# Kernel optimization log

Measured on AMD Instinct MI355X. Metric: run time of the kernel, lower is better.

## Reference

```python
import jax, jax.numpy as jnp
import numpy as np

D_MODEL = 1024
NUM_HEADS = 16
DEPTH = D_MODEL // NUM_HEADS
MAX_SEQ = 2048
B, S = 2, 2048


def setup_inputs() -> dict:
    key = jax.random.key(0)
    ks = jax.random.split(key, 12)
    scale = 1.0 / np.sqrt(D_MODEL)
    inp = {
        'q': jax.random.normal(ks[0], (B, S, D_MODEL), jnp.float32),
        'k': jax.random.normal(ks[1], (B, S, D_MODEL), jnp.float32),
        'v': jax.random.normal(ks[2], (B, S, D_MODEL), jnp.float32),
        'mask': jnp.zeros((B, 1, S, S), jnp.float32),
        'wq_w': jax.random.normal(ks[3], (D_MODEL, D_MODEL), jnp.float32) * scale,
        'wq_b': jnp.zeros((D_MODEL,), jnp.float32),
        'wk_w': jax.random.normal(ks[4], (D_MODEL, D_MODEL), jnp.float32) * scale,
        'wk_b': jnp.zeros((D_MODEL,), jnp.float32),
        'wv_w': jax.random.normal(ks[5], (D_MODEL, D_MODEL), jnp.float32) * scale,
        'wv_b': jnp.zeros((D_MODEL,), jnp.float32),
        'dense_w': jax.random.normal(ks[6], (D_MODEL, D_MODEL), jnp.float32) * scale,
        'dense_b': jnp.zeros((D_MODEL,), jnp.float32),
        'rel_bias': jax.random.normal(ks[7], (2 * MAX_SEQ - 1, NUM_HEADS), jnp.float32),
    }
    return inp


def _split_heads(x):
    # [B, S, D_MODEL] -> [B, H, S, depth]
    b, s, _ = x.shape
    return x.reshape(b, s, NUM_HEADS, DEPTH).transpose(0, 2, 1, 3)


def reference(q, k, v, mask, wq_w, wq_b, wk_w, wk_b, wv_w, wv_b, dense_w, dense_b, rel_bias):
    b, s, _ = q.shape
    # torch Linear: y = x @ W.T + b
    qh = _split_heads(q @ wq_w.T + wq_b)
    kh = _split_heads(k @ wk_w.T + wk_b)
    vh = _split_heads(v @ wv_w.T + wv_b)
    logits = jnp.einsum('bhqd,bhkd->bhqk', qh, kh) / jnp.sqrt(jnp.float32(DEPTH))
    # relative position bias gather
    pos = jnp.arange(s)
    idx = jnp.clip(pos[:, None] - pos[None, :] + MAX_SEQ - 1, 0, 2 * MAX_SEQ - 2)  # [S, S]
    pos_bias = rel_bias[idx]                      # [S, S, H]
    pos_bias = pos_bias.transpose(2, 0, 1)[None]  # [1, H, S, S]
    logits = logits + pos_bias + mask * (-1e9)
    attn = jax.nn.softmax(logits, axis=-1)        # dropout is identity in eval
    out = jnp.einsum('bhqk,bhkd->bhqd', attn, vh)
    out = out.transpose(0, 2, 1, 3).reshape(b, s, D_MODEL)
    out = out @ dense_w.T + dense_b
    return out, attn
```

## Files before the change

kernel.cpp:

```cpp
#include <hip/hip_runtime.h>

typedef _Float16 f16x8 __attribute__((ext_vector_type(8)));
typedef _Float16 f16x4 __attribute__((ext_vector_type(4)));
typedef float f32x4 __attribute__((ext_vector_type(4)));
typedef unsigned short u16x8 __attribute__((ext_vector_type(8)));
typedef unsigned int u32;

#define MFMA16H(a, b, c) __builtin_amdgcn_mfma_f32_16x16x32_f16(a, b, c, 0, 0, 0)

#if __has_builtin(__builtin_amdgcn_exp2f)
#define EXP2F(x) __builtin_amdgcn_exp2f(x)
#else
#define EXP2F(x) exp2f(x)
#endif

#define LOG2E 1.44269504088896340736f
#define SHIFT2 5.0f

__device__ __forceinline__ unsigned short f2bf(float x) {
  unsigned u = __float_as_uint(x);
  u += 0x7FFF + ((u >> 16) & 1);
  return (unsigned short)(u >> 16);
}
__device__ __forceinline__ float bf2f(unsigned short h) {
  return __uint_as_float(((unsigned)h) << 16);
}
__device__ __forceinline__ f16x8 ldh8(const _Float16* p) {
  return *reinterpret_cast<const f16x8*>(p);
}
__device__ __forceinline__ u16x8 ldu8(const unsigned short* p) {
  return *reinterpret_cast<const u16x8*>(p);
}

__global__ __launch_bounds__(256) void prep_kernel(
    const float* __restrict__ q, const float* __restrict__ k, const float* __restrict__ v,
    const float* __restrict__ wq, const float* __restrict__ wk, const float* __restrict__ wv,
    const float* __restrict__ dwt, const float* __restrict__ mask,
    _Float16* __restrict__ qf, _Float16* __restrict__ kf, _Float16* __restrict__ vf,
    _Float16* __restrict__ wqf, _Float16* __restrict__ wkf, _Float16* __restrict__ wvf,
    _Float16* __restrict__ dwf, unsigned short* __restrict__ mperm) {
  if (blockIdx.x < 2048) {
    const int blk = blockIdx.x;
    const int kt = blk & 31, bq = blk >> 5;
    const int b = bq >> 5, qt = bq & 31;
    const int lane = threadIdx.x;
    const int w = lane >> 6, lg = (lane >> 4) & 3, lr = lane & 15;
    const int q0 = qt * 64;
    const float cs = -1e9f * LOG2E;
    unsigned short vals[16];
#pragma unroll
    for (int c = 0; c < 4; ++c)
#pragma unroll
      for (int r = 0; r < 4; ++r) {
        const int qr = q0 + w * 16 + lg * 4 + r;
        const int kc = kt * 64 + c * 16 + lr;
        vals[c * 4 + r] = f2bf(mask[((size_t)b * 2048 + qr) * 2048 + kc] * cs);
      }
    uint4* out = reinterpret_cast<uint4*>(mperm) + ((size_t)blk * 256 + lane) * 2;
    out[0] = *reinterpret_cast<uint4*>(&vals[0]);
    out[1] = *reinterpret_cast<uint4*>(&vals[8]);
    return;
  }
  const int i = (blockIdx.x - 2048) * 256 + threadIdx.x;
  const int r = i >> 18;
  const int j = i & 262143;
  const float* src;
  _Float16* dst;
  int off = 0;
  if (r < 4)       { src = q;   dst = qf;  off = r * 262144; }
  else if (r < 8)  { src = k;   dst = kf;  off = (r - 4) * 262144; }
  else if (r < 12) { src = v;   dst = vf;  off = (r - 8) * 262144; }
  else if (r == 12){ src = wq;  dst = wqf; }
  else if (r == 13){ src = wk;  dst = wkf; }
  else if (r == 14){ src = wv;  dst = wvf; }
  else             { src = dwt; dst = dwf; }
  const int g = off + j;
  float4 x = reinterpret_cast<const float4*>(src)[g];
  f16x4 h;
  h[0] = (_Float16)x.x; h[1] = (_Float16)x.y;
  h[2] = (_Float16)x.z; h[3] = (_Float16)x.w;
  reinterpret_cast<f16x4*>(dst)[g] = h;
}

__device__ __forceinline__ void gemm_body(
    int t, int mode, const _Float16* __restrict__ A, const _Float16* __restrict__ B,
    const float* __restrict__ bias, _Float16* __restrict__ out_h, float* __restrict__ out_f,
    _Float16* As, _Float16* Bs) {
  const int tid = threadIdx.x;
  const int tm = t & 31, tn = t >> 5;
  const int m0 = tm * 128, n0 = tn * 128;
  const int w = tid >> 6, l = tid & 63, lg = l >> 4, lr = l & 15;
  const int wr = w >> 1, wc = w & 1;
  const int srow = tid >> 2, scol = (tid & 3) * 8;

  f32x4 acc[4][4] = {};

  for (int kt = 0; kt < 32; ++kt) {
    const int k0 = kt * 32;
    uint4 ra[2], rb[2];
#pragma unroll
    for (int it = 0; it < 2; ++it) {
      const int row = it * 64 + srow;
      ra[it] = *reinterpret_cast<const uint4*>(A + (size_t)(m0 + row) * 1024 + k0 + scol);
      rb[it] = *reinterpret_cast<const uint4*>(B + (size_t)(n0 + row) * 1024 + k0 + scol);
    }
    __syncthreads();
#pragma unroll
    for (int it = 0; it < 2; ++it) {
      const int eo = (it * 256 + tid) * 8;
      *reinterpret_cast<uint4*>(As + eo) = ra[it];
      *reinterpret_cast<uint4*>(Bs + eo) = rb[it];
    }
    __syncthreads();

    f16x8 fa[4], fb[4];
#pragma unroll
    for (int i = 0; i < 4; ++i) {
      fa[i] = ldh8(As + (wr * 64 + i * 16 + lr) * 32 + lg * 8);
      fb[i] = ldh8(Bs + (wc * 64 + i * 16 + lr) * 32 + lg * 8);
    }
#pragma unroll
    for (int i = 0; i < 4; ++i)
#pragma unroll
      for (int j = 0; j < 4; ++j)
        acc[i][j] = MFMA16H(fa[i], fb[j], acc[i][j]);
  }

#pragma unroll
  for (int i = 0; i < 4; ++i) {
    const int mrow = m0 + wr * 64 + i * 16 + lg * 4;
#pragma unroll
    for (int j = 0; j < 4; ++j) {
      const int ncol = n0 + wc * 64 + j * 16 + lr;
      const float bv = bias[ncol];
#pragma unroll
      for (int r = 0; r < 4; ++r) {
        const int m = mrow + r;
        const float v = acc[i][j][r] + bv;
        if (mode == 2) {
          out_f[(size_t)m * 1024 + ncol] = v;
        } else {
          const int bb = m >> 11, s = m & 2047, hh = ncol >> 6, d = ncol & 63;
          if (mode == 0)
            out_h[((size_t)(bb * 16 + hh) * 2048 + s) * 64 + d] = (_Float16)v;
          else
            out_h[((size_t)(bb * 16 + hh) * 64 + d) * 2048 + s] = (_Float16)v;
        }
      }
    }
  }
}

__global__ __launch_bounds__(256, 3) void proj_gemm_kernel(
    const _Float16* __restrict__ qf, const _Float16* __restrict__ kf, const _Float16* __restrict__ vf,
    const _Float16* __restrict__ wqf, const _Float16* __restrict__ wkf, const _Float16* __restrict__ wvf,
    const float* __restrict__ bq, const float* __restrict__ bk, const float* __restrict__ bv,
    _Float16* __restrict__ qhf, _Float16* __restrict__ khf, _Float16* __restrict__ vhT) {
  __shared__ __align__(16) _Float16 As[128 * 32];
  __shared__ __align__(16) _Float16 Bs[128 * 32];
  const int mode = blockIdx.x >> 8;
  const int t = blockIdx.x & 255;
  if (mode == 0)      gemm_body(t, 0, qf, wqf, bq, qhf, nullptr, As, Bs);
  else if (mode == 1) gemm_body(t, 0, kf, wkf, bk, khf, nullptr, As, Bs);
  else                gemm_body(t, 1, vf, wvf, bv, vhT, nullptr, As, Bs);
}

__global__ __launch_bounds__(256) void dense_gemm_kernel(
    const _Float16* __restrict__ A, const _Float16* __restrict__ Bw,
    const float* __restrict__ bias, float* __restrict__ out_f) {
  __shared__ __align__(16) _Float16 As[128 * 32];
  __shared__ __align__(16) _Float16 Bs[128 * 32];
  gemm_body(blockIdx.x, 2, A, Bw, bias, nullptr, out_f, As, Bs);
}

__global__ __launch_bounds__(128) void attn_sums_kernel(
    const _Float16* __restrict__ qh, const _Float16* __restrict__ kh,
    const float* __restrict__ rel_bias, const unsigned short* __restrict__ mperm,
    float* __restrict__ sums2) {
  __shared__ float rb2[2080];
  const int bid = blockIdx.x;
  const int wg = ((bid & 7) << 9) | (bid >> 3);
  const int half = wg & 1;
  const int qt = (wg >> 1) & 63;
  const int bh = wg >> 7;
  const int b = bh >> 4, h = bh & 15;
  const int q0 = qt * 32;
  const int tid = threadIdx.x;
  const int w2 = tid >> 6, l = tid & 63, lg = l >> 4, lr = l & 15;

  for (int t = tid; t < 2079; t += 128)
    rb2[t] = rel_bias[(q0 + t) * 16 + h] * LOG2E - SHIFT2;

  const size_t bh_off = (size_t)bh * 2048 * 64;
  const _Float16* qhb = qh + bh_off;
  const _Float16* khb = kh + bh_off;
  const int qt64 = qt >> 1;
  const int wp = (qt & 1) * 2 + w2;
  const int lanep = wp * 64 + lg * 16 + lr;
  const unsigned short* mpb =
      mperm + (((size_t)(b * 32 + qt64) * 32) * 256 + lanep) * 16;

  f16x8 qf[2];
  {
    const size_t qrow = (size_t)(q0 + w2 * 16 + lr) * 64;
    qf[0] = ldh8(qhb + qrow + lg * 8);
    qf[1] = ldh8(qhb + qrow + 32 + lg * 8);
  }
  __syncthreads();

  const int qbase = w2 * 16 + lg * 4;
  const float c1 = 0.125f * LOG2E;
  float sacc[4] = {0.f, 0.f, 0.f, 0.f};

  const int kt0 = half * 16;
#pragma unroll 2
  for (int kt = kt0; kt < kt0 + 16; ++kt) {
    u16x8 m0v = ldu8(mpb + (size_t)kt * 4096);
    u16x8 m1v = ldu8(mpb + (size_t)kt * 4096 + 8);
#pragma unroll
    for (int c = 0; c < 4; ++c) {
      const int kc = kt * 64 + c * 16 + lr;
      const _Float16* kr = khb + (size_t)kc * 64 + lg * 8;
      f32x4 acc = {};
      acc = MFMA16H(qf[0], ldh8(kr), acc);
      acc = MFMA16H(qf[1], ldh8(kr + 32), acc);
#pragma unroll
      for (int r = 0; r < 4; ++r) {
        const float mbf = bf2f((c < 2) ? (unsigned short)m0v[(c & 1) * 4 + r]
                                       : (unsigned short)m1v[(c & 1) * 4 + r]);
        const float l2 = fmaf(acc[r], c1, rb2[qbase + r - kc + 2047]) + mbf;
        sacc[r] += EXP2F(l2);
      }
    }
  }

#pragma unroll
  for (int r = 0; r < 4; ++r) {
    float s = sacc[r];
    s += __shfl_xor(s, 1);
    s += __shfl_xor(s, 2);
    s += __shfl_xor(s, 4);
    s += __shfl_xor(s, 8);
    if (lr == 0)
      sums2[((size_t)bh * 2048 + q0 + qbase + r) * 2 + half] = s;
  }
}

__global__ __launch_bounds__(128) void attn_emit_kernel(
    const _Float16* __restrict__ qh, const _Float16* __restrict__ kh,
    const _Float16* __restrict__ vT,
    const float* __restrict__ rel_bias, const unsigned short* __restrict__ mperm,
    const float* __restrict__ sums2, float* __restrict__ attn_out,
    _Float16* __restrict__ o_h) {
  __shared__ float rb2[2080];
  __shared__ __align__(16) _Float16 p16t[2][32 * 76];

  const int bid = blockIdx.x;
  const int wg = ((bid & 7) << 8) | (bid >> 3);
  const int qt = wg & 63;
  const int bh = wg >> 6;
  const int b = bh >> 4, h = bh & 15;
  const int q0 = qt * 32;
  const int tid = threadIdx.x;
  const int w2 = tid >> 6, l = tid & 63, lg = l >> 4, lr = l & 15;

  for (int t = tid; t < 2079; t += 128)
    rb2[t] = rel_bias[(q0 + t) * 16 + h] * LOG2E - SHIFT2;

  const size_t bh_off = (size_t)bh * 2048 * 64;
  const _Float16* qhb = qh + bh_off;
  const _Float16* khb = kh + bh_off;
  const _Float16* vTb = vT + bh_off;
  const int qt64 = qt >> 1;
  const int wp = (qt & 1) * 2 + w2;
  const int lanep = wp * 64 + lg * 16 + lr;
  const unsigned short* mpb =
      mperm + (((size_t)(b * 32 + qt64) * 32) * 256 + lanep) * 16;
  float* attn_bh = attn_out + (size_t)bh * 2048 * 2048;

  const int qbase = w2 * 16 + lg * 4;

  f16x8 qf[2];
  {
    const size_t qrow = (size_t)(q0 + w2 * 16 + lr) * 64;
    qf[0] = ldh8(qhb + qrow + lg * 8);
    qf[1] = ldh8(qhb + qrow + 32 + lg * 8);
  }
  float inv[4];
  {
    const float* sp = sums2 + ((size_t)bh * 2048 + q0 + qbase) * 2;
    float4 s0 = *reinterpret_cast<const float4*>(sp);
    float4 s1 = *reinterpret_cast<const float4*>(sp + 4);
    inv[0] = 1.0f / (s0.x + s0.y);
    inv[1] = 1.0f / (s0.z + s0.w);
    inv[2] = 1.0f / (s1.x + s1.y);
    inv[3] = 1.0f / (s1.z + s1.w);
  }
  __syncthreads();

  const float c1 = 0.125f * LOG2E;
  f32x4 acc_o[4] = {};
  const int sg = l >> 4, sc = (l & 15) * 4;

#pragma unroll 2
  for (int kt = 0; kt < 32; ++kt) {
    _Float16* tile = p16t[kt & 1];
    u16x8 m0v = ldu8(mpb + (size_t)kt * 4096);
    u16x8 m1v = ldu8(mpb + (size_t)kt * 4096 + 8);
#pragma unroll
    for (int c = 0; c < 4; ++c) {
      const int kc = kt * 64 + c * 16 + lr;
      const _Float16* kr = khb + (size_t)kc * 64 + lg * 8;
      f32x4 acc = {};
      acc = MFMA16H(qf[0], ldh8(kr), acc);
      acc = MFMA16H(qf[1], ldh8(kr + 32), acc);
#pragma unroll
      for (int r = 0; r < 4; ++r) {
        const float mbf = bf2f((c < 2) ? (unsigned short)m0v[(c & 1) * 4 + r]
                                       : (unsigned short)m1v[(c & 1) * 4 + r]);
        const float l2 = fmaf(acc[r], c1, rb2[qbase + r - kc + 2047]) + mbf;
        tile[(qbase + r) * 76 + c * 16 + lr] = (_Float16)(EXP2F(l2) * inv[r]);
      }
    }
    f16x8 pf0 = ldh8(tile + (w2 * 16 + lr) * 76 + lg * 8);
    f16x8 pf1 = ldh8(tile + (w2 * 16 + lr) * 76 + 32 + lg * 8);
#pragma unroll
    for (int n = 0; n < 4; ++n) {
      const _Float16* vr = vTb + (size_t)(n * 16 + lr) * 2048 + kt * 64 + lg * 8;
      acc_o[n] = MFMA16H(pf0, ldh8(vr), acc_o[n]);
      acc_o[n] = MFMA16H(pf1, ldh8(vr + 32), acc_o[n]);
    }
#pragma unroll
    for (int i = 0; i < 4; ++i) {
      const int row = w2 * 16 + i * 4 + sg;
      f16x4 pw = *reinterpret_cast<const f16x4*>(tile + row * 76 + sc);
      float4 o;
      o.x = (float)pw[0]; o.y = (float)pw[1];
      o.z = (float)pw[2]; o.w = (float)pw[3];
      *reinterpret_cast<float4*>(attn_bh + (size_t)(q0 + row) * 2048 + kt * 64 + sc) = o;
    }
  }

#pragma unroll
  for (int n = 0; n < 4; ++n)
#pragma unroll
    for (int r = 0; r < 4; ++r) {
      const int qr = q0 + qbase + r;
      const int d = n * 16 + lr;
      o_h[((size_t)(b * 2048 + qr) * 16 + h) * 64 + d] = (_Float16)acc_o[n][r];
    }
}

extern "C" void kernel_launch(void* const* d_in, const int* in_sizes, int n_in,
                              void* d_out, int out_size, void* d_ws, size_t ws_size,
                              hipStream_t stream) {
  const float* q = (const float*)d_in[0];
  const float* k = (const float*)d_in[1];
  const float* v = (const float*)d_in[2];
  const float* mask = (const float*)d_in[3];
  const float* wq_w = (const float*)d_in[4];
  const float* wq_b = (const float*)d_in[5];
  const float* wk_w = (const float*)d_in[6];
  const float* wk_b = (const float*)d_in[7];
  const float* wv_w = (const float*)d_in[8];
  const float* wv_b = (const float*)d_in[9];
  const float* dw = (const float*)d_in[10];
  const float* db = (const float*)d_in[11];
  const float* rel = (const float*)d_in[12];

  char* ws = (char*)d_ws;
  _Float16* qf_in = (_Float16*)(ws + 0);
  _Float16* kf_in = (_Float16*)(ws + 8388608);
  _Float16* vf_in = (_Float16*)(ws + 16777216);
  _Float16* wqf   = (_Float16*)(ws + 25165824);
  _Float16* wkf   = (_Float16*)(ws + 27262976);
  _Float16* wvf   = (_Float16*)(ws + 29360128);
  _Float16* dwf   = (_Float16*)(ws + 31457280);
  _Float16* qhf   = (_Float16*)(ws + 33554432);
  _Float16* khf   = (_Float16*)(ws + 41943040);
  _Float16* vhT   = (_Float16*)(ws + 50331648);
  _Float16* o_h   = (_Float16*)(ws + 58720256);
  float* sums2    = (float*)(ws + 67108864);
  unsigned short* mperm = (unsigned short*)(ws + 67633152);

  float* out = (float*)d_out;
  float* attn_out = out + 4194304;

  prep_kernel<<<18432, 256, 0, stream>>>(q, k, v, wq_w, wk_w, wv_w, dw, mask,
                                         qf_in, kf_in, vf_in, wqf, wkf, wvf, dwf, mperm);

  proj_gemm_kernel<<<768, 256, 0, stream>>>(qf_in, kf_in, vf_in, wqf, wkf, wvf,
                                            wq_b, wk_b, wv_b, qhf, khf, vhT);

  attn_sums_kernel<<<4096, 128, 0, stream>>>(qhf, khf, rel, mperm, sums2);

  attn_emit_kernel<<<2048, 128, 0, stream>>>(qhf, khf, vhT, rel, mperm,
                                             sums2, attn_out, o_h);

  dense_gemm_kernel<<<256, 256, 0, stream>>>(o_h, dwf, db, out);
}
```

Baseline: 681.4 us.

## Precompute permuted fp16 relative-bias tiles and split attention emit across key halves

Relative-position bias is precomputed in the prep kernel into per-head, per-diagonal fp16 tiles laid out in MFMA lane order. Both attention kernels add these tiles to the fp16 mask tiles instead of staging a float bias table in LDS, which removes LDS fills and one sync per block. The emit kernel now uses 256-thread blocks over 64 query rows, each handling one half of the keys, and writes partial outputs to two buffers. The dense GEMM sums those buffers while loading A. The risks are lost precision from fp16 bias, mask and partial outputs, the removed SHIFT2 offset, and extra workspace traffic.

```diff
diff --git a/kernel.cpp b/kernel.cpp
--- a/kernel.cpp
+++ b/kernel.cpp
@@ -3,7 +3,6 @@
 typedef _Float16 f16x8 __attribute__((ext_vector_type(8)));
 typedef _Float16 f16x4 __attribute__((ext_vector_type(4)));
 typedef float f32x4 __attribute__((ext_vector_type(4)));
-typedef unsigned short u16x8 __attribute__((ext_vector_type(8)));
 typedef unsigned int u32;
 
 #define MFMA16H(a, b, c) __builtin_amdgcn_mfma_f32_16x16x32_f16(a, b, c, 0, 0, 0)
@@ -15,53 +14,58 @@
 #endif
 
 #define LOG2E 1.44269504088896340736f
-#define SHIFT2 5.0f
-
-__device__ __forceinline__ unsigned short f2bf(float x) {
-  unsigned u = __float_as_uint(x);
-  u += 0x7FFF + ((u >> 16) & 1);
-  return (unsigned short)(u >> 16);
-}
-__device__ __forceinline__ float bf2f(unsigned short h) {
-  return __uint_as_float(((unsigned)h) << 16);
-}
+
 __device__ __forceinline__ f16x8 ldh8(const _Float16* p) {
   return *reinterpret_cast<const f16x8*>(p);
-}
-__device__ __forceinline__ u16x8 ldu8(const unsigned short* p) {
-  return *reinterpret_cast<const u16x8*>(p);
 }
 
 __global__ __launch_bounds__(256) void prep_kernel(
     const float* __restrict__ q, const float* __restrict__ k, const float* __restrict__ v,
     const float* __restrict__ wq, const float* __restrict__ wk, const float* __restrict__ wv,
-    const float* __restrict__ dwt, const float* __restrict__ mask,
+    const float* __restrict__ dwt, const float* __restrict__ mask, const float* __restrict__ rel,
     _Float16* __restrict__ qf, _Float16* __restrict__ kf, _Float16* __restrict__ vf,
     _Float16* __restrict__ wqf, _Float16* __restrict__ wkf, _Float16* __restrict__ wvf,
-    _Float16* __restrict__ dwf, unsigned short* __restrict__ mperm) {
+    _Float16* __restrict__ dwf, _Float16* __restrict__ mperm, _Float16* __restrict__ rperm) {
+  const int lane = threadIdx.x;
+  const int w = lane >> 6, lg = (lane >> 4) & 3, lr = lane & 15;
   if (blockIdx.x < 2048) {
     const int blk = blockIdx.x;
     const int kt = blk & 31, bq = blk >> 5;
     const int b = bq >> 5, qt = bq & 31;
-    const int lane = threadIdx.x;
-    const int w = lane >> 6, lg = (lane >> 4) & 3, lr = lane & 15;
     const int q0 = qt * 64;
     const float cs = -1e9f * LOG2E;
-    unsigned short vals[16];
+    _Float16 vals[16];
 #pragma unroll
     for (int c = 0; c < 4; ++c)
 #pragma unroll
       for (int r = 0; r < 4; ++r) {
         const int qr = q0 + w * 16 + lg * 4 + r;
         const int kc = kt * 64 + c * 16 + lr;
-        vals[c * 4 + r] = f2bf(mask[((size_t)b * 2048 + qr) * 2048 + kc] * cs);
+        vals[c * 4 + r] =
+            (_Float16)fmaxf(mask[((size_t)b * 2048 + qr) * 2048 + kc] * cs, -60000.0f);
       }
     uint4* out = reinterpret_cast<uint4*>(mperm) + ((size_t)blk * 256 + lane) * 2;
     out[0] = *reinterpret_cast<uint4*>(&vals[0]);
     out[1] = *reinterpret_cast<uint4*>(&vals[8]);
     return;
   }
-  const int i = (blockIdx.x - 2048) * 256 + threadIdx.x;
+  if (blockIdx.x < 3056) {
+    const int blk = blockIdx.x - 2048;
+    const int h = blk / 63, d = blk % 63;
+    _Float16 vals[16];
+#pragma unroll
+    for (int c = 0; c < 4; ++c)
+#pragma unroll
+      for (int r = 0; r < 4; ++r) {
+        const int idx = (d - 31) * 64 + (w * 16 + lg * 4 + r) - (c * 16 + lr) + 2047;
+        vals[c * 4 + r] = (_Float16)(rel[idx * 16 + h] * LOG2E);
+      }
+    uint4* out = reinterpret_cast<uint4*>(rperm) + ((size_t)blk * 256 + lane) * 2;
+    out[0] = *reinterpret_cast<uint4*>(&vals[0]);
+    out[1] = *reinterpret_cast<uint4*>(&vals[8]);
+    return;
+  }
+  const int i = (blockIdx.x - 3056) * 256 + threadIdx.x;
   const int r = i >> 18;
   const int j = i & 262143;
   const float* src;
@@ -76,10 +80,10 @@
   else             { src = dwt; dst = dwf; }
   const int g = off + j;
   float4 x = reinterpret_cast<const float4*>(src)[g];
-  f16x4 h;
-  h[0] = (_Float16)x.x; h[1] = (_Float16)x.y;
-  h[2] = (_Float16)x.z; h[3] = (_Float16)x.w;
-  reinterpret_cast<f16x4*>(dst)[g] = h;
+  f16x4 h4;
+  h4[0] = (_Float16)x.x; h4[1] = (_Float16)x.y;
+  h4[2] = (_Float16)x.z; h4[3] = (_Float16)x.w;
+  reinterpret_cast<f16x4*>(dst)[g] = h4;
 }
 
 __device__ __forceinline__ void gemm_body(
@@ -166,18 +170,71 @@
 }
 
 __global__ __launch_bounds__(256) void dense_gemm_kernel(
-    const _Float16* __restrict__ A, const _Float16* __restrict__ Bw,
-    const float* __restrict__ bias, float* __restrict__ out_f) {
+    const _Float16* __restrict__ A0, const _Float16* __restrict__ A1,
+    const _Float16* __restrict__ Bw, const float* __restrict__ bias,
+    float* __restrict__ out_f) {
   __shared__ __align__(16) _Float16 As[128 * 32];
   __shared__ __align__(16) _Float16 Bs[128 * 32];
-  gemm_body(blockIdx.x, 2, A, Bw, bias, nullptr, out_f, As, Bs);
-}
-
-__global__ __launch_bounds__(128) void attn_sums_kernel(
+  const int tid = threadIdx.x;
+  const int t = blockIdx.x;
+  const int tm = t & 31, tn = t >> 5;
+  const int m0 = tm * 128, n0 = tn * 128;
+  const int w = tid >> 6, l = tid & 63, lg = l >> 4, lr = l & 15;
+  const int wr = w >> 1, wc = w & 1;
+  const int srow = tid >> 2, scol = (tid & 3) * 8;
+
+  f32x4 acc[4][4] = {};
+
+  for (int kt = 0; kt < 32; ++kt) {
+    const int k0 = kt * 32;
+    f16x8 ra[2], rb[2];
+#pragma unroll
+    for (int it = 0; it < 2; ++it) {
+      const int row = it * 64 + srow;
+      const size_t ga = (size_t)(m0 + row) * 1024 + k0 + scol;
+      ra[it] = ldh8(A0 + ga) + ldh8(A1 + ga);
+      rb[it] = ldh8(Bw + (size_t)(n0 + row) * 1024 + k0 + scol);
+    }
+    __syncthreads();
+#pragma unroll
+    for (int it = 0; it < 2; ++it) {
+      const int eo = (it * 256 + tid) * 8;
+      *reinterpret_cast<f16x8*>(As + eo) = ra[it];
+      *reinterpret_cast<f16x8*>(Bs + eo) = rb[it];
+    }
+    __syncthreads();
+
+    f16x8 fa[4], fb[4];
+#pragma unroll
+    for (int i = 0; i < 4; ++i) {
+      fa[i] = ldh8(As + (wr * 64 + i * 16 + lr) * 32 + lg * 8);
+      fb[i] = ldh8(Bs + (wc * 64 + i * 16 + lr) * 32 + lg * 8);
+    }
+#pragma unroll
+    for (int i = 0; i < 4; ++i)
+#pragma unroll
+      for (int j = 0; j < 4; ++j)
+        acc[i][j] = MFMA16H(fa[i], fb[j], acc[i][j]);
+  }
+
+#pragma unroll
+  for (int i = 0; i < 4; ++i) {
+    const int mrow = m0 + wr * 64 + i * 16 + lg * 4;
+#pragma unroll
+    for (int j = 0; j < 4; ++j) {
+      const int ncol = n0 + wc * 64 + j * 16 + lr;
+      const float bv = bias[ncol];
+#pragma unroll
+      for (int r = 0; r < 4; ++r)
+        out_f[(size_t)(mrow + r) * 1024 + ncol] = acc[i][j][r] + bv;
+    }
+  }
+}
+
+__global__ __launch_bounds__(128, 8) void attn_sums_kernel(
     const _Float16* __restrict__ qh, const _Float16* __restrict__ kh,
-    const float* __restrict__ rel_bias, const unsigned short* __restrict__ mperm,
+    const _Float16* __restrict__ mperm, const _Float16* __restrict__ rperm,
     float* __restrict__ sums2) {
-  __shared__ float rb2[2080];
   const int bid = blockIdx.x;
   const int wg = ((bid & 7) << 9) | (bid >> 3);
   const int half = wg & 1;
@@ -188,25 +245,21 @@
   const int tid = threadIdx.x;
   const int w2 = tid >> 6, l = tid & 63, lg = l >> 4, lr = l & 15;
 
-  for (int t = tid; t < 2079; t += 128)
-    rb2[t] = rel_bias[(q0 + t) * 16 + h] * LOG2E - SHIFT2;
-
   const size_t bh_off = (size_t)bh * 2048 * 64;
   const _Float16* qhb = qh + bh_off;
   const _Float16* khb = kh + bh_off;
   const int qt64 = qt >> 1;
   const int wp = (qt & 1) * 2 + w2;
   const int lanep = wp * 64 + lg * 16 + lr;
-  const unsigned short* mpb =
-      mperm + (((size_t)(b * 32 + qt64) * 32) * 256 + lanep) * 16;
-
-  f16x8 qf[2];
+  const _Float16* mpb = mperm + ((size_t)(b * 32 + qt64) * 32 * 256 + lanep) * 16;
+  const _Float16* rpb = rperm + ((size_t)(h * 63 + qt64 + 31) * 256 + lanep) * 16;
+
+  f16x8 qfr[2];
   {
     const size_t qrow = (size_t)(q0 + w2 * 16 + lr) * 64;
-    qf[0] = ldh8(qhb + qrow + lg * 8);
-    qf[1] = ldh8(qhb + qrow + 32 + lg * 8);
-  }
-  __syncthreads();
+    qfr[0] = ldh8(qhb + qrow + lg * 8);
+    qfr[1] = ldh8(qhb + qrow + 32 + lg * 8);
+  }
 
   const int qbase = w2 * 16 + lg * 4;
   const float c1 = 0.125f * LOG2E;
@@ -215,21 +268,19 @@
   const int kt0 = half * 16;
 #pragma unroll 2
   for (int kt = kt0; kt < kt0 + 16; ++kt) {
-    u16x8 m0v = ldu8(mpb + (size_t)kt * 4096);
-    u16x8 m1v = ldu8(mpb + (size_t)kt * 4096 + 8);
+    f16x8 b0 = ldh8(mpb + (size_t)kt * 4096) + ldh8(rpb - (size_t)kt * 4096);
+    f16x8 b1 = ldh8(mpb + (size_t)kt * 4096 + 8) + ldh8(rpb - (size_t)kt * 4096 + 8);
 #pragma unroll
     for (int c = 0; c < 4; ++c) {
       const int kc = kt * 64 + c * 16 + lr;
       const _Float16* kr = khb + (size_t)kc * 64 + lg * 8;
       f32x4 acc = {};
-      acc = MFMA16H(qf[0], ldh8(kr), acc);
-      acc = MFMA16H(qf[1], ldh8(kr + 32), acc);
+      acc = MFMA16H(qfr[0], ldh8(kr), acc);
+      acc = MFMA16H(qfr[1], ldh8(kr + 32), acc);
 #pragma unroll
       for (int r = 0; r < 4; ++r) {
-        const float mbf = bf2f((c < 2) ? (unsigned short)m0v[(c & 1) * 4 + r]
-                                       : (unsigned short)m1v[(c & 1) * 4 + r]);
-        const float l2 = fmaf(acc[r], c1, rb2[qbase + r - kc + 2047]) + mbf;
-        sacc[r] += EXP2F(l2);
+        const float bias = (float)((c < 2) ? b0[(c & 1) * 4 + r] : b1[(c & 1) * 4 + r]);
+        sacc[r] += EXP2F(fmaf(acc[r], c1, bias));
       }
     }
   }
@@ -246,45 +297,40 @@
   }
 }
 
-__global__ __launch_bounds__(128) void attn_emit_kernel(
+__global__ __launch_bounds__(256, 8) void attn_emit_kernel(
     const _Float16* __restrict__ qh, const _Float16* __restrict__ kh,
     const _Float16* __restrict__ vT,
-    const float* __restrict__ rel_bias, const unsigned short* __restrict__ mperm,
+    const _Float16* __restrict__ mperm, const _Float16* __restrict__ rperm,
     const float* __restrict__ sums2, float* __restrict__ attn_out,
-    _Float16* __restrict__ o_h) {
-  __shared__ float rb2[2080];
-  __shared__ __align__(16) _Float16 p16t[2][32 * 76];
+    _Float16* __restrict__ o0, _Float16* __restrict__ o1) {
+  __shared__ __align__(16) _Float16 p16t[2][64 * 76];
 
   const int bid = blockIdx.x;
   const int wg = ((bid & 7) << 8) | (bid >> 3);
-  const int qt = wg & 63;
+  const int khalf = wg & 1;
+  const int qt64 = (wg >> 1) & 31;
   const int bh = wg >> 6;
   const int b = bh >> 4, h = bh & 15;
-  const int q0 = qt * 32;
+  const int q0 = qt64 * 64;
   const int tid = threadIdx.x;
-  const int w2 = tid >> 6, l = tid & 63, lg = l >> 4, lr = l & 15;
-
-  for (int t = tid; t < 2079; t += 128)
-    rb2[t] = rel_bias[(q0 + t) * 16 + h] * LOG2E - SHIFT2;
+  const int w = tid >> 6, l = tid & 63, lg = l >> 4, lr = l & 15;
 
   const size_t bh_off = (size_t)bh * 2048 * 64;
   const _Float16* qhb = qh + bh_off;
   const _Float16* khb = kh + bh_off;
   const _Float16* vTb = vT + bh_off;
-  const int qt64 = qt >> 1;
-  const int wp = (qt & 1) * 2 + w2;
-  const int lanep = wp * 64 + lg * 16 + lr;
-  const unsigned short* mpb =
-      mperm + (((size_t)(b * 32 + qt64) * 32) * 256 + lanep) * 16;
+  const _Float16* mpb = mperm + ((size_t)(b * 32 + qt64) * 32 * 256 + tid) * 16;
+  const _Float16* rpb = rperm + ((size_t)(h * 63 + qt64 + 31) * 256 + tid) * 16;
   float* attn_bh = attn_out + (size_t)bh * 2048 * 2048;
-
-  const int qbase = w2 * 16 + lg * 4;
-
-  f16x8 qf[2];
+  _Float16* opart = khalf ? o1 : o0;
+
+  const int qbase = w * 16 + lg * 4;
+
+  f16x8 qfr[2];
   {
-    const size_t qrow = (size_t)(q0 + w2 * 16 + lr) * 64;
-    qf[0] = ldh8(qhb + qrow + lg * 8);
-    qf[1] = ldh8(qhb + qrow + 32 + lg * 8);
+    const size_t qrow = (size_t)(q0 + w * 16 + lr) * 64;
+    qfr[0] = ldh8(qhb + qrow + lg * 8);
+    qfr[1] = ldh8(qhb + qrow + 32 + lg * 8);
   }
   float inv[4];
   {
@@ -296,48 +342,49 @@
     inv[2] = 1.0f / (s1.x + s1.y);
     inv[3] = 1.0f / (s1.z + s1.w);
   }
-  __syncthreads();
 
   const float c1 = 0.125f * LOG2E;
   f32x4 acc_o[4] = {};
-  const int sg = l >> 4, sc = (l & 15) * 4;
-
+  const int srow = w * 16 + (l >> 2);
+  const int scb = (l & 3) * 16;
+  const float invr = 0.0f;
+
+  const int kt0 = khalf * 16;
 #pragma unroll 2
-  for (int kt = 0; kt < 32; ++kt) {
+  for (int kt = kt0; kt < kt0 + 16; ++kt) {
     _Float16* tile = p16t[kt & 1];
-    u16x8 m0v = ldu8(mpb + (size_t)kt * 4096);
-    u16x8 m1v = ldu8(mpb + (size_t)kt * 4096 + 8);
+    f16x8 b0 = ldh8(mpb + (size_t)kt * 4096) + ldh8(rpb - (size_t)kt * 4096);
+    f16x8 b1 = ldh8(mpb + (size_t)kt * 4096 + 8) + ldh8(rpb - (size_t)kt * 4096 + 8);
 #pragma unroll
     for (int c = 0; c < 4; ++c) {
       const int kc = kt * 64 + c * 16 + lr;
       const _Float16* kr = khb + (size_t)kc * 64 + lg * 8;
       f32x4 acc = {};
-      acc = MFMA16H(qf[0], ldh8(kr), acc);
-      acc = MFMA16H(qf[1], ldh8(kr + 32), acc);
+      acc = MFMA16H(qfr[0], ldh8(kr), acc);
+      acc = MFMA16H(qfr[1], ldh8(kr + 32), acc);
 #pragma unroll
       for (int r = 0; r < 4; ++r) {
-        const float mbf = bf2f((c < 2) ? (unsigned short)m0v[(c & 1) * 4 + r]
-                                       : (unsigned short)m1v[(c & 1) * 4 + r]);
-        const float l2 = fmaf(acc[r], c1, rb2[qbase + r - kc + 2047]) + mbf;
-        tile[(qbase + r) * 76 + c * 16 + lr] = (_Float16)(EXP2F(l2) * inv[r]);
+        const float bias = (float)((c < 2) ? b0[(c & 1) * 4 + r] : b1[(c & 1) * 4 + r]);
+        tile[(qbase + r) * 76 + c * 16 + lr] =
+            (_Float16)(EXP2F(fmaf(acc[r], c1, bias)) * inv[r]);
       }
     }
-    f16x8 pf0 = ldh8(tile + (w2 * 16 + lr) * 76 + lg * 8);
-    f16x8 pf1 = ldh8(tile + (w2 * 16 + lr) * 76 + 32 + lg * 8);
+    f16x8 pf0 = ldh8(tile + (w * 16 + lr) * 76 + lg * 8);
+    f16x8 pf1 = ldh8(tile + (w * 16 + lr) * 76 + 32 + lg * 8);
 #pragma unroll
     for (int n = 0; n < 4; ++n) {
       const _Float16* vr = vTb + (size_t)(n * 16 + lr) * 2048 + kt * 64 + lg * 8;
       acc_o[n] = MFMA16H(pf0, ldh8(vr), acc_o[n]);
       acc_o[n] = MFMA16H(pf1, ldh8(vr + 32), acc_o[n]);
     }
+    float* arow = attn_bh + (size_t)(q0 + srow) * 2048 + kt * 64 + scb;
 #pragma unroll
     for (int i = 0; i < 4; ++i) {
-      const int row = w2 * 16 + i * 4 + sg;
-      f16x4 pw = *reinterpret_cast<const f16x4*>(tile + row * 76 + sc);
+      f16x4 pw = *reinterpret_cast<const f16x4*>(tile + srow * 76 + scb + i * 4);
       float4 o;
       o.x = (float)pw[0]; o.y = (float)pw[1];
       o.z = (float)pw[2]; o.w = (float)pw[3];
-      *reinterpret_cast<float4*>(attn_bh + (size_t)(q0 + row) * 2048 + kt * 64 + sc) = o;
+      *reinterpret_cast<float4*>(arow + i * 4) = o;
     }
   }
 
@@ -347,7 +394,7 @@
     for (int r = 0; r < 4; ++r) {
       const int qr = q0 + qbase + r;
       const int d = n * 16 + lr;
-      o_h[((size_t)(b * 2048 + qr) * 16 + h) * 64 + d] = (_Float16)acc_o[n][r];
+      opart[((size_t)(b * 2048 + qr) * 16 + h) * 64 + d] = (_Float16)acc_o[n][r];
     }
 }
 
@@ -379,23 +426,26 @@
   _Float16* qhf   = (_Float16*)(ws + 33554432);
   _Float16* khf   = (_Float16*)(ws + 41943040);
   _Float16* vhT   = (_Float16*)(ws + 50331648);
-  _Float16* o_h   = (_Float16*)(ws + 58720256);
-  float* sums2    = (float*)(ws + 67108864);
-  unsigned short* mperm = (unsigned short*)(ws + 67633152);
+  _Float16* o0    = (_Float16*)(ws + 58720256);
+  _Float16* o1    = (_Float16*)(ws + 67108864);
+  float* sums2    = (float*)(ws + 75497472);
+  _Float16* mperm = (_Float16*)(ws + 76021760);
+  _Float16* rperm = (_Float16*)(ws + 92798976);
 
   float* out = (float*)d_out;
   float* attn_out = out + 4194304;
 
-  prep_kernel<<<18432, 256, 0, stream>>>(q, k, v, wq_w, wk_w, wv_w, dw, mask,
-                                         qf_in, kf_in, vf_in, wqf, wkf, wvf, dwf, mperm);
+  prep_kernel<<<19440, 256, 0, stream>>>(q, k, v, wq_w, wk_w, wv_w, dw, mask, rel,
+                                         qf_in, kf_in, vf_in, wqf, wkf, wvf, dwf,
+                                         mperm, rperm);
 
   proj_gemm_kernel<<<768, 256, 0, stream>>>(qf_in, kf_in, vf_in, wqf, wkf, wvf,
                                             wq_b, wk_b, wv_b, qhf, khf, vhT);
 
-  attn_sums_kernel<<<4096, 128, 0, stream>>>(qhf, khf, rel, mperm, sums2);
-
-  attn_emit_kernel<<<2048, 128, 0, stream>>>(qhf, khf, vhT, rel, mperm,
-                                             sums2, attn_out, o_h);
-
-  dense_gemm_kernel<<<256, 256, 0, stream>>>(o_h, dwf, db, out);
-}
+  attn_sums_kernel<<<4096, 128, 0, stream>>>(qhf, khf, mperm, rperm, sums2);
+
+  attn_emit_kernel<<<2048, 256, 0, stream>>>(qhf, khf, vhT, mperm, rperm,
+                                             sums2, attn_out, o0, o1);
+
+  dense_gemm_kernel<<<256, 256, 0, stream>>>(o0, o1, dwf, db, out);
+}
```

After: 857.4 us. 25.8% more time.
